# Optimization experiments

Hardware: AMD Instinct MI355X
Metric: run time of the kernel (lower is better)

The kernel has to match this reference:

```python
import jax, jax.numpy as jnp
import numpy as np

B_, N_, DIM, MDIM, H, HID = 8, 1024, 256, 128, 8, 1024
HD = DIM // H      # 32
MHD = MDIM // H    # 16
EPS = 1e-5


def _bn(x, g, b):
    # x: [B, C, L]; BatchNorm1d with batch statistics (training-mode fwd), biased var
    m = x.mean(axis=(0, 2), keepdims=True)
    v = x.var(axis=(0, 2), keepdims=True)
    return (x - m) / jnp.sqrt(v + EPS) * g[None, :, None] + b[None, :, None]


def setup_inputs() -> dict:
    key = jax.random.key(0)
    ks = jax.random.split(key, 12)
    p = lambda k, s: 0.02 * jax.random.normal(k, s, dtype=jnp.float32)
    z = lambda n: jnp.zeros((n,), jnp.float32)
    return {
        "x": jax.random.normal(ks[0], (B_, DIM, N_), dtype=jnp.float32),
        "cor": jax.random.uniform(ks[1], (B_, N_, 3), dtype=jnp.float32),
        "q_w": p(ks[2], (DIM, DIM)),            # qkv_bias=False
        "kv_w": p(ks[3], (2 * DIM, DIM)),
        "cor_w": p(ks[4], (MDIM, 3)),
        "proj_w": p(ks[5], (DIM, DIM)), "proj_b": z(DIM),
        "mproj_w": p(ks[6], (MDIM, MDIM)), "mproj_b": z(MDIM),
        "g1": jnp.ones((DIM,), jnp.float32), "b1": z(DIM),
        "g2": jnp.ones((DIM,), jnp.float32), "b2": z(DIM),
        "fc1_w": p(ks[7], (HID, DIM)), "fc1_b": z(HID),
        "dw_w": 1.0 + p(ks[8], (HID,)), "dw_b": z(HID),  # Conv1d k=1 groups=C -> per-channel affine
        "prelu_a": jnp.array(0.25, jnp.float32),
        "fc2_w": p(ks[9], (DIM, HID)), "fc2_b": z(DIM),
        "N": N_,
        "B": B_,
    }


def reference(x, cor, q_w, kv_w, cor_w, proj_w, proj_b, mproj_w, mproj_b,
              g1, b1, g2, b2, fc1_w, fc1_b, dw_w, dw_b, prelu_a,
              fc2_w, fc2_b, N, B):
    nwB = x.shape[0]
    scale = float(HD) ** -0.5
    # norm1 + to tokens [B, N, C]
    xn = _bn(x, g1, b1).transpose(0, 2, 1)
    # swap batch halves (frame reversal)
    xr = jnp.concatenate([xn[nwB // 2:], xn[:nwB // 2]], axis=0)
    # attention projections
    q = (xn @ q_w.T).reshape(nwB, N_, H, HD).transpose(0, 2, 1, 3)       # [B,H,N,hd]
    kv = (xr @ kv_w.T).reshape(nwB, N_, 2, H, HD).transpose(2, 0, 3, 1, 4)
    k, v = kv[0], kv[1]
    ce = cor @ cor_w.T                                                    # [B,N,M]
    ceh = ce.reshape(nwB, N_, H, MHD).transpose(0, 2, 1, 3)               # [B,H,N,mhd]
    attn = jax.nn.softmax(jnp.einsum('bhnd,bhmd->bhnm', q, k) * scale, axis=-1)
    # attention matrix reused for value and motion paths
    xa = (attn @ v).transpose(0, 2, 1, 3).reshape(nwB, N_, DIM) @ proj_w.T + proj_b
    cr = (attn @ ceh).transpose(0, 2, 1, 3).reshape(nwB, N_, MDIM)
    motion = (cr - ce) @ mproj_w.T + mproj_b
    # residual + norm2 + DWConv-MLP
    xn2 = xn + xa                                                         # [B,N,C]
    xb = _bn(xn2.transpose(0, 2, 1), g2, b2).transpose(0, 2, 1)           # [B,N,C]
    h = xb @ fc1_w.T + fc1_b
    h = h * dw_w + dw_b                                                   # depthwise 1x1 conv
    h = jnp.where(h >= 0, h, prelu_a * h)                                 # PReLU
    out = h @ fc2_w.T + fc2_b
    x_out = x + out.transpose(0, 2, 1)                                    # [B,C,N]
    return (x_out, motion)
```

## Files before the change

### kernel.cpp

```cpp
#include <hip/hip_runtime.h>
#include <hip/hip_bf16.h>
#include <math.h>

#define C_DIM 256
#define N_PTS 1024
#define H_N 8
#define MDIM_N 128
#define HID_N 1024
#define EPSV 1e-5f
#define R_TOT 8192
#define CN 262144

typedef __bf16 bf16x8 __attribute__((ext_vector_type(8)));
typedef __bf16 bf16x4 __attribute__((ext_vector_type(4)));
typedef float f32x4 __attribute__((ext_vector_type(4)));

#define QSCALE 0.25503482f

__device__ inline unsigned short bfu(float f) {
  union { __bf16 h; unsigned short u; } c;
  c.h = (__bf16)f;
  return c.u;
}

__global__ __launch_bounds__(256)
void wcvt_k(const float* __restrict__ s0, const float* __restrict__ s1,
            const float* __restrict__ s2, const float* __restrict__ s3,
            const float* __restrict__ s4, const float* __restrict__ s5,
            __bf16* d0, __bf16* d1, __bf16* d2, __bf16* d3, __bf16* d4,
            __bf16* d5) {
  int i = blockIdx.x * 256 + threadIdx.x;
  const float* s; __bf16* d; int off;
  if      (i <  16384) { s = s0; d = d0; off = 0; }
  else if (i <  49152) { s = s1; d = d1; off = 16384; }
  else if (i <  65536) { s = s2; d = d2; off = 49152; }
  else if (i <  69632) { s = s3; d = d3; off = 65536; }
  else if (i < 135168) { s = s4; d = d4; off = 69632; }
  else                 { s = s5; d = d5; off = 135168; }
  int j = i - off;
  float4 v = ((const float4*)s)[j];
  ushort4 u;
  u.x = bfu(v.x); u.y = bfu(v.y); u.z = bfu(v.z); u.w = bfu(v.w);
  ((ushort4*)d)[j] = u;
}

__global__ __launch_bounds__(256)
void bn1_stats_k(const float* __restrict__ x, const float* __restrict__ g,
                 const float* __restrict__ bb, float* __restrict__ st) {
  int c = blockIdx.x;
  int t = threadIdx.x;
  float s = 0.f, q = 0.f;
  for (int i = 0; i < 32; ++i) {
    int idx = t + i * 256;
    int b = idx >> 10, n = idx & 1023;
    float v = x[(size_t)b * CN + (size_t)c * N_PTS + n];
    s += v; q += v * v;
  }
  __shared__ float ss[256], sq[256];
  ss[t] = s; sq[t] = q;
  __syncthreads();
  for (int off = 128; off > 0; off >>= 1) {
    if (t < off) { ss[t] += ss[t + off]; sq[t] += sq[t + off]; }
    __syncthreads();
  }
  if (t == 0) {
    float mean = ss[0] * (1.f / 8192.f);
    float var  = sq[0] * (1.f / 8192.f) - mean * mean;
    float sc   = g[c] * rsqrtf(var + EPSV);
    st[c]          = sc;
    st[C_DIM + c]  = bb[c] - mean * sc;
  }
}

__global__ __launch_bounds__(256)
void norm1_t_k(const float* __restrict__ x, const float* __restrict__ st,
               float* __restrict__ xn, __bf16* __restrict__ xnb) {
  __shared__ float tile[32][33];
  int c0 = blockIdx.x * 32, n0 = blockIdx.y * 32, b = blockIdx.z;
  int tx = threadIdx.x, ty = threadIdx.y;
#pragma unroll
  for (int k = 0; k < 4; ++k) {
    int ci = ty + k * 8;
    int c = c0 + ci;
    float v = x[(size_t)b * CN + (size_t)c * N_PTS + n0 + tx];
    tile[ci][tx] = v * st[c] + st[C_DIM + c];
  }
  __syncthreads();
#pragma unroll
  for (int k = 0; k < 4; ++k) {
    int ni = ty + k * 8;
    size_t o = ((size_t)(b * N_PTS + n0 + ni)) * C_DIM + c0 + tx;
    float v = tile[tx][ni];
    xn[o] = v;
    xnb[o] = (__bf16)v;
  }
}

__global__ __launch_bounds__(256)
void cet_k(const float* __restrict__ cor, const float* __restrict__ cw,
           __bf16* __restrict__ vt) {
  __shared__ float cs[768];
  int bh = blockIdx.x; int b = bh >> 3, h = bh & 7;
  int n0 = blockIdx.y * 256;
  int t = threadIdx.x;
  for (int i = t; i < 768; i += 256)
    cs[i] = cor[(size_t)(b * N_PTS + n0) * 3 + i];
  __syncthreads();
  int md = t >> 4, ns = (t & 15) * 16;
  float w0 = cw[(h * 16 + md) * 3 + 0];
  float w1 = cw[(h * 16 + md) * 3 + 1];
  float w2 = cw[(h * 16 + md) * 3 + 2];
  __bf16* dst = &vt[((size_t)bh * 48 + 32 + md) * 1024 + n0 + ns];
#pragma unroll
  for (int g2 = 0; g2 < 4; ++g2) {
    ushort4 u;
    float v0 = cs[(ns + g2 * 4 + 0) * 3] * w0 + cs[(ns + g2 * 4 + 0) * 3 + 1] * w1 + cs[(ns + g2 * 4 + 0) * 3 + 2] * w2;
    float v1 = cs[(ns + g2 * 4 + 1) * 3] * w0 + cs[(ns + g2 * 4 + 1) * 3 + 1] * w1 + cs[(ns + g2 * 4 + 1) * 3 + 2] * w2;
    float v2 = cs[(ns + g2 * 4 + 2) * 3] * w0 + cs[(ns + g2 * 4 + 2) * 3 + 1] * w1 + cs[(ns + g2 * 4 + 2) * 3 + 2] * w2;
    float v3 = cs[(ns + g2 * 4 + 3) * 3] * w0 + cs[(ns + g2 * 4 + 3) * 3 + 1] * w1 + cs[(ns + g2 * 4 + 3) * 3 + 2] * w2;
    u.x = bfu(v0); u.y = bfu(v1); u.z = bfu(v2); u.w = bfu(v3);
    *(ushort4*)&dst[g2 * 4] = u;
  }
}

__global__ __launch_bounds__(512)
void attn_k(const __bf16* __restrict__ qb, const __bf16* __restrict__ kb,
            const __bf16* __restrict__ vt, const float* __restrict__ cor,
            const float* __restrict__ cw, __bf16* __restrict__ av,
            __bf16* __restrict__ dmc) {
  __shared__ __bf16 KsV[2][64][40];
  __shared__ __bf16 VtV[2][48][72];
  __shared__ __bf16 Pbuf[8][16][72];

  int bh = blockIdx.x; int b = bh >> 3, h = bh & 7;
  int t = threadIdx.x;
  int w = t >> 6, lane = t & 63;
  int l15 = lane & 15, g = lane >> 4;

  int nloc0 = blockIdx.y * 128 + w * 16;
  bf16x8 aq =
      *(const bf16x8*)&qb[((size_t)bh * N_PTS + nloc0 + l15) * 32 + g * 8];

  const __bf16* ksrc = kb + (size_t)bh * N_PTS * 32;
  const __bf16* vsrc = vt + (size_t)bh * 48 * N_PTS;
  int u = t - 256;
  int vdv = u >> 3, vkg = u & 7;

  float mrun = -1e30f, lrun = 0.f;
  f32x4 acco[3];
#pragma unroll
  for (int mt = 0; mt < 3; ++mt) acco[mt] = (f32x4){0.f, 0.f, 0.f, 0.f};

  if (t < 256) {
    *(uint4*)&KsV[0][t >> 2][(t & 3) * 8] = *(const uint4*)&ksrc[t * 8];
  } else {
    *(uint4*)&VtV[0][vdv][vkg * 8] =
        *(const uint4*)&vsrc[(size_t)vdv * N_PTS + vkg * 8];
    if (u < 128)
      *(uint4*)&VtV[0][32 + vdv][vkg * 8] =
          *(const uint4*)&vsrc[(size_t)(32 + vdv) * N_PTS + vkg * 8];
  }
  __syncthreads();

  for (int kt = 0; kt < 16; ++kt) {
    int cur = kt & 1, nxt = cur ^ 1;
    uint4 kreg, vreg0, vreg1;
    if (kt < 15) {
      int key1 = (kt + 1) * 64;
      if (t < 256) {
        kreg = *(const uint4*)&ksrc[key1 * 32 + t * 8];
      } else {
        vreg0 = *(const uint4*)&vsrc[(size_t)vdv * N_PTS + key1 + vkg * 8];
        if (u < 128)
          vreg1 =
              *(const uint4*)&vsrc[(size_t)(32 + vdv) * N_PTS + key1 + vkg * 8];
      }
    }

    f32x4 sq[4];
    __builtin_amdgcn_s_setprio(1);
#pragma unroll
    for (int nt = 0; nt < 4; ++nt) {
      bf16x8 kf = *(const bf16x8*)&KsV[cur][nt * 16 + l15][g * 8];
      f32x4 z = (f32x4){0.f, 0.f, 0.f, 0.f};
      sq[nt] = __builtin_amdgcn_mfma_f32_16x16x32_bf16(kf, aq, z, 0, 0, 0);
    }
    __builtin_amdgcn_s_setprio(0);

    float tm = fmaxf(fmaxf(fmaxf(sq[0][0], sq[0][1]), fmaxf(sq[0][2], sq[0][3])),
                     fmaxf(fmaxf(sq[1][0], sq[1][1]), fmaxf(sq[1][2], sq[1][3])));
    tm = fmaxf(tm,
               fmaxf(fmaxf(fmaxf(sq[2][0], sq[2][1]), fmaxf(sq[2][2], sq[2][3])),
                     fmaxf(fmaxf(sq[3][0], sq[3][1]), fmaxf(sq[3][2], sq[3][3]))));
    tm = fmaxf(tm, __shfl_xor(tm, 16));
    tm = fmaxf(tm, __shfl_xor(tm, 32));
    float nm = fmaxf(mrun, tm);
    float corr = exp2f(mrun - nm);
    mrun = nm;
    float rs = 0.f;
#pragma unroll
    for (int nt = 0; nt < 4; ++nt)
#pragma unroll
      for (int r = 0; r < 4; ++r) {
        float p = exp2f(sq[nt][r] - nm);
        sq[nt][r] = p;
        rs += p;
      }
    rs += __shfl_xor(rs, 16);
    rs += __shfl_xor(rs, 32);
    lrun = lrun * corr + rs;
#pragma unroll
    for (int mt = 0; mt < 3; ++mt)
#pragma unroll
      for (int r = 0; r < 4; ++r) acco[mt][r] *= corr;

#pragma unroll
    for (int nt = 0; nt < 4; ++nt) {
      bf16x4 pk;
      pk[0] = (__bf16)sq[nt][0]; pk[1] = (__bf16)sq[nt][1];
      pk[2] = (__bf16)sq[nt][2]; pk[3] = (__bf16)sq[nt][3];
      *(bf16x4*)&Pbuf[w][l15][nt * 16 + g * 4] = pk;
    }
    bf16x8 ap[2];
#pragma unroll
    for (int kc = 0; kc < 2; ++kc)
      ap[kc] = *(const bf16x8*)&Pbuf[w][l15][kc * 32 + g * 8];

    __builtin_amdgcn_s_setprio(1);
#pragma unroll
    for (int mt = 0; mt < 3; ++mt)
#pragma unroll
      for (int kc = 0; kc < 2; ++kc) {
        bf16x8 vf = *(const bf16x8*)&VtV[cur][mt * 16 + l15][kc * 32 + g * 8];
        acco[mt] = __builtin_amdgcn_mfma_f32_16x16x32_bf16(vf, ap[kc],
                                                           acco[mt], 0, 0, 0);
      }
    __builtin_amdgcn_s_setprio(0);

    if (kt < 15) {
      if (t < 256) {
        *(uint4*)&KsV[nxt][t >> 2][(t & 3) * 8] = kreg;
      } else {
        *(uint4*)&VtV[nxt][vdv][vkg * 8] = vreg0;
        if (u < 128) *(uint4*)&VtV[nxt][32 + vdv][vkg * 8] = vreg1;
      }
      __syncthreads();
    }
  }

  float inv = 1.f / lrun;
  int row = b * N_PTS + nloc0 + l15;
#pragma unroll
  for (int mt = 0; mt < 2; ++mt) {
    ushort4 o;
    o.x = bfu(acco[mt][0] * inv); o.y = bfu(acco[mt][1] * inv);
    o.z = bfu(acco[mt][2] * inv); o.w = bfu(acco[mt][3] * inv);
    *(ushort4*)&av[(size_t)row * C_DIM + h * 32 + mt * 16 + g * 4] = o;
  }
  {
    const float* cp = &cor[(size_t)row * 3];
    float c0 = cp[0], c1 = cp[1], c2 = cp[2];
    ushort4 o;
#pragma unroll
    for (int r = 0; r < 4; ++r) {
      int md = h * 16 + g * 4 + r;
      float ce = c0 * cw[md * 3] + c1 * cw[md * 3 + 1] + c2 * cw[md * 3 + 2];
      float v = acco[2][r] * inv - ce;
      ((unsigned short*)&o)[r] = bfu(v);
    }
    *(ushort4*)&dmc[(size_t)row * MDIM_N + h * 16 + g * 4] = o;
  }
}

template <int MODE, int BNt>
__global__ __launch_bounds__(256)
void mgemm_k(const __bf16* __restrict__ A, const __bf16* __restrict__ W,
             const float* __restrict__ bias, void* __restrict__ outp,
             const float* __restrict__ e0, const float* __restrict__ e2,
             const float* __restrict__ e3, const float* __restrict__ pre,
             __bf16* __restrict__ kbp, __bf16* __restrict__ vtp,
             float* __restrict__ raw2, int K, int M) {
  constexpr int WN = BNt / 2;
  constexpr int NR = WN / 16;
  __shared__ __bf16 Al[128 * 64];
  __shared__ __bf16 Bl[BNt * 64];
  int t = threadIdx.x;
  int w = t >> 6, lane = t & 63;
  int l15 = lane & 15, g = lane >> 4;
  int wr = w >> 1, wn = w & 1;
  int r0 = blockIdx.y * 128;
  int m0 = blockIdx.x * BNt;
  bool swapA = (MODE == 1) && (m0 >= 256);

  f32x4 acc[4][NR];
#pragma unroll
  for (int i = 0; i < 4; ++i)
#pragma unroll
    for (int j = 0; j < NR; ++j) acc[i][j] = (f32x4){0.f, 0.f, 0.f, 0.f};

  for (int kt = 0; kt < K; kt += 64) {
    __syncthreads();
#pragma unroll
    for (int p = 0; p < 4; ++p) {
      int flat = p * 256 + t;
      int row = flat >> 3, c16 = flat & 7;
      int gr = r0 + row;
      if (swapA) gr = ((((gr >> 10) + 4) & 7) << 10) | (gr & 1023);
      *(uint4*)&Al[row * 64 + (c16 ^ (row & 7)) * 8] =
          *(const uint4*)&A[(size_t)gr * K + kt + c16 * 8];
    }
#pragma unroll
    for (int p = 0; p < BNt / 32; ++p) {
      int flat = p * 256 + t;
      int row = flat >> 3, c16 = flat & 7;
      *(uint4*)&Bl[row * 64 + (c16 ^ (row & 7)) * 8] =
          *(const uint4*)&W[(size_t)(m0 + row) * K + kt + c16 * 8];
    }
    __syncthreads();
#pragma unroll
    for (int ks = 0; ks < 2; ++ks) {
      bf16x8 af[4], bf_[NR];
#pragma unroll
      for (int mf = 0; mf < 4; ++mf) {
        int row = wr * 64 + mf * 16 + l15;
        af[mf] = *(const bf16x8*)&Al[row * 64 + ((ks * 4 + g) ^ (l15 & 7)) * 8];
      }
#pragma unroll
      for (int nf = 0; nf < NR; ++nf) {
        int row = wn * WN + nf * 16 + l15;
        bf_[nf] = *(const bf16x8*)&Bl[row * 64 + ((ks * 4 + g) ^ (l15 & 7)) * 8];
      }
#pragma unroll
      for (int mf = 0; mf < 4; ++mf)
#pragma unroll
        for (int nf = 0; nf < NR; ++nf)
          acc[mf][nf] = __builtin_amdgcn_mfma_f32_16x16x32_bf16(
              af[mf], bf_[nf], acc[mf][nf], 0, 0, 0);
    }
  }

  float a_pre = (MODE == 4) ? pre[0] : 0.f;
  float sS[NR], sQ[NR];
#pragma unroll
  for (int j = 0; j < NR; ++j) { sS[j] = 0.f; sQ[j] = 0.f; }

#pragma unroll
  for (int mf = 0; mf < 4; ++mf) {
#pragma unroll
    for (int nf = 0; nf < NR; ++nf) {
      int m = m0 + wn * WN + nf * 16 + l15;
      int rbase = r0 + wr * 64 + mf * 16 + g * 4;
      if (MODE == 5) {
        int b = rbase >> 10, n = rbase & 1023;
        size_t oi = (size_t)b * CN + (size_t)m * N_PTS + n;
        float4 xv = *(const float4*)&e0[oi];
        float bs = bias[m];
        float4 ov;
        ov.x = xv.x + acc[mf][nf][0] + bs;
        ov.y = xv.y + acc[mf][nf][1] + bs;
        ov.z = xv.z + acc[mf][nf][2] + bs;
        ov.w = xv.w + acc[mf][nf][3] + bs;
        *(float4*)&((float*)outp)[oi] = ov;
      } else if (MODE == 1 && m0 >= 512) {
        int d = m - 512, hh = d >> 5, dd = d & 31;
        int b = rbase >> 10, n0v = rbase & 1023;
        ushort4 uu;
        uu.x = bfu(acc[mf][nf][0]); uu.y = bfu(acc[mf][nf][1]);
        uu.z = bfu(acc[mf][nf][2]); uu.w = bfu(acc[mf][nf][3]);
        *(ushort4*)&vtp[(((size_t)b * 8 + hh) * 48 + dd) * 1024 + n0v] = uu;
      } else {
#pragma unroll
        for (int r = 0; r < 4; ++r) {
          float v = acc[mf][nf][r];
          if (MODE == 1) {
            int b = rbase >> 10, n = (rbase & 1023) + r;
            if (m0 < 256) {
              int hh = m >> 5, dd = m & 31;
              ((__bf16*)outp)[(((size_t)b * 8 + hh) * 1024 + n) * 32 + dd] =
                  (__bf16)(v * QSCALE);
            } else {
              int d = m - 256, hh = d >> 5, dd = d & 31;
              kbp[(((size_t)b * 8 + hh) * 1024 + n) * 32 + dd] = (__bf16)v;
            }
          } else if (MODE == 2) {
            size_t oi = (size_t)(rbase + r) * M + m;
            float vv = e0[oi] + v + bias[m];
            ((float*)outp)[oi] = vv;
            sS[nf] += vv;
            sQ[nf] += vv * vv;
          } else if (MODE == 3) {
            ((float*)outp)[(size_t)(rbase + r) * M + m] = v + bias[m];
          } else if (MODE == 4) {
            v += bias[m];
            v = v * e2[m] + e3[m];
            ((__bf16*)outp)[(size_t)(rbase + r) * M + m] =
                (__bf16)(v >= 0.f ? v : a_pre * v);
          }
        }
      }
    }
  }

  if (MODE == 2) {
    __syncthreads();
    float* colS = (float*)&Al[0];
    float* colQ = colS + BNt;
    if (t < 2 * BNt) colS[t] = 0.f;
    __syncthreads();
#pragma unroll
    for (int nf = 0; nf < NR; ++nf) {
      int mc = wn * WN + nf * 16 + l15;
      atomicAdd(&colS[mc], sS[nf]);
      atomicAdd(&colQ[mc], sQ[nf]);
    }
    __syncthreads();
    if (t < BNt) {
      atomicAdd(&raw2[m0 + t], colS[t]);
      atomicAdd(&raw2[256 + m0 + t], colQ[t]);
    }
  }
}

__global__ __launch_bounds__(256)
void bn2af_k(const float* __restrict__ xn2, const float* __restrict__ raw,
             const float* __restrict__ g, const float* __restrict__ bb,
             __bf16* __restrict__ xb) {
  __shared__ float sts[256], sth[256];
  int t = threadIdx.x;
  {
    float mean = raw[t] * (1.f / 8192.f);
    float var  = raw[256 + t] * (1.f / 8192.f) - mean * mean;
    float sc   = g[t] * rsqrtf(var + EPSV);
    sts[t] = sc;
    sth[t] = bb[t] - mean * sc;
  }
  __syncthreads();
  int i = blockIdx.x * 256 + t;
  float4 v = ((const float4*)xn2)[i];
  int c = (i * 4) & 255;
  ushort4 u;
  u.x = bfu(v.x * sts[c]     + sth[c]);
  u.y = bfu(v.y * sts[c + 1] + sth[c + 1]);
  u.z = bfu(v.z * sts[c + 2] + sth[c + 2]);
  u.w = bfu(v.w * sts[c + 3] + sth[c + 3]);
  ((ushort4*)xb)[i] = u;
}

extern "C" void kernel_launch(void* const* d_in, const int* in_sizes, int n_in,
                              void* d_out, int out_size, void* d_ws,
                              size_t ws_size, hipStream_t stream) {
  const float* x       = (const float*)d_in[0];
  const float* cor     = (const float*)d_in[1];
  const float* q_w     = (const float*)d_in[2];
  const float* kv_w    = (const float*)d_in[3];
  const float* cor_w   = (const float*)d_in[4];
  const float* proj_w  = (const float*)d_in[5];
  const float* proj_b  = (const float*)d_in[6];
  const float* mproj_w = (const float*)d_in[7];
  const float* mproj_b = (const float*)d_in[8];
  const float* g1      = (const float*)d_in[9];
  const float* b1      = (const float*)d_in[10];
  const float* g2      = (const float*)d_in[11];
  const float* b2      = (const float*)d_in[12];
  const float* fc1_w   = (const float*)d_in[13];
  const float* fc1_b   = (const float*)d_in[14];
  const float* dw_w    = (const float*)d_in[15];
  const float* dw_b    = (const float*)d_in[16];
  const float* prelu   = (const float*)d_in[17];
  const float* fc2_w   = (const float*)d_in[18];
  const float* fc2_b   = (const float*)d_in[19];

  char* base = (char*)d_ws;
  const size_t MB = 1u << 20;
  float*  xn32 = (float*)(base + 0);
  __bf16* xnb  = (__bf16*)(base + 8 * MB);
  __bf16* qb   = (__bf16*)(base + 12 * MB);
  __bf16* kb   = (__bf16*)(base + 16 * MB);
  __bf16* vt   = (__bf16*)(base + 20 * MB);
  __bf16* av   = (__bf16*)(base + 30 * MB);
  __bf16* dmc  = (__bf16*)(base + 34 * MB);
  float*  xn2  = (float*)(base + 36 * MB);
  __bf16* xb   = (__bf16*)(base + 8 * MB);
  __bf16* hb   = (__bf16*)(base + 12 * MB);
  __bf16* qwb  = (__bf16*)(base + 44 * MB);
  __bf16* kvwb = (__bf16*)(base + 44 * MB + 131072);
  __bf16* pwb  = (__bf16*)(base + 44 * MB + 393216);
  __bf16* mwb  = (__bf16*)(base + 44 * MB + 524288);
  __bf16* f1wb = (__bf16*)(base + 44 * MB + 557056);
  __bf16* f2wb = (__bf16*)(base + 44 * MB + 1081344);
  float*  raw2 = (float*)(base + 45 * MB + 655360);
  float*  st1  = raw2 + 1024;
  float* out0 = (float*)d_out;
  float* out1 = out0 + 2097152;

  (void)hipMemsetAsync(raw2, 0, 512 * sizeof(float), stream);

  wcvt_k<<<784, 256, 0, stream>>>(q_w, kv_w, proj_w, mproj_w, fc1_w, fc2_w,
                                  qwb, kvwb, pwb, mwb, f1wb, f2wb);
  bn1_stats_k<<<256, 256, 0, stream>>>(x, g1, b1, st1);
  norm1_t_k<<<dim3(8, 32, 8), dim3(32, 8), 0, stream>>>(x, st1, xn32, xnb);

  mgemm_k<1, 128><<<dim3(6, 64), 256, 0, stream>>>(
      xnb, qwb, nullptr, qb, nullptr, nullptr, nullptr, nullptr, kb, vt,
      nullptr, 256, 768);
  cet_k<<<dim3(64, 4), 256, 0, stream>>>(cor, cor_w, vt);

  attn_k<<<dim3(64, 8), 512, 0, stream>>>(qb, kb, vt, cor, cor_w, av, dmc);

  mgemm_k<2, 64><<<dim3(4, 64), 256, 0, stream>>>(
      av, pwb, proj_b, xn2, xn32, nullptr, nullptr, nullptr, nullptr, nullptr,
      raw2, 256, 256);
  mgemm_k<3, 64><<<dim3(2, 64), 256, 0, stream>>>(
      dmc, mwb, mproj_b, out1, nullptr, nullptr, nullptr, nullptr, nullptr,
      nullptr, nullptr, 128, 128);

  bn2af_k<<<2048, 256, 0, stream>>>(xn2, raw2, g2, b2, xb);

  mgemm_k<4, 128><<<dim3(8, 64), 256, 0, stream>>>(
      xb, f1wb, fc1_b, hb, nullptr, dw_w, dw_b, prelu, nullptr, nullptr,
      nullptr, 256, HID_N);
  mgemm_k<5, 64><<<dim3(4, 64), 256, 0, stream>>>(
      hb, f2wb, fc2_b, out0, x, nullptr, nullptr, nullptr, nullptr, nullptr,
      nullptr, HID_N, 256);
}
```

Before: 119.3 us.

## Fuse prep kernels, merge proj/motion GEMMs, fold BN2 into fc1 loader

```diff
diff --git a/kernel.cpp b/kernel.cpp
--- a/kernel.cpp
+++ b/kernel.cpp
@@ -24,57 +24,82 @@
 }
 
 __global__ __launch_bounds__(256)
-void wcvt_k(const float* __restrict__ s0, const float* __restrict__ s1,
+void prep_k(const float* __restrict__ s0, const float* __restrict__ s1,
             const float* __restrict__ s2, const float* __restrict__ s3,
             const float* __restrict__ s4, const float* __restrict__ s5,
             __bf16* d0, __bf16* d1, __bf16* d2, __bf16* d3, __bf16* d4,
-            __bf16* d5) {
-  int i = blockIdx.x * 256 + threadIdx.x;
-  const float* s; __bf16* d; int off;
-  if      (i <  16384) { s = s0; d = d0; off = 0; }
-  else if (i <  49152) { s = s1; d = d1; off = 16384; }
-  else if (i <  65536) { s = s2; d = d2; off = 49152; }
-  else if (i <  69632) { s = s3; d = d3; off = 65536; }
-  else if (i < 135168) { s = s4; d = d4; off = 69632; }
-  else                 { s = s5; d = d5; off = 135168; }
-  int j = i - off;
-  float4 v = ((const float4*)s)[j];
-  ushort4 u;
-  u.x = bfu(v.x); u.y = bfu(v.y); u.z = bfu(v.z); u.w = bfu(v.w);
-  ((ushort4*)d)[j] = u;
-}
-
-__global__ __launch_bounds__(256)
-void bn1_stats_k(const float* __restrict__ x, const float* __restrict__ g,
-                 const float* __restrict__ bb, float* __restrict__ st) {
-  int c = blockIdx.x;
+            __bf16* d5, const float* __restrict__ cor,
+            const float* __restrict__ cw, __bf16* __restrict__ vt,
+            const float* __restrict__ x, const float* __restrict__ g1,
+            const float* __restrict__ b1, float* __restrict__ st) {
+  int blk = blockIdx.x;
   int t = threadIdx.x;
-  float s = 0.f, q = 0.f;
-  for (int i = 0; i < 32; ++i) {
-    int idx = t + i * 256;
-    int b = idx >> 10, n = idx & 1023;
-    float v = x[(size_t)b * CN + (size_t)c * N_PTS + n];
-    s += v; q += v * v;
-  }
-  __shared__ float ss[256], sq[256];
-  ss[t] = s; sq[t] = q;
-  __syncthreads();
-  for (int off = 128; off > 0; off >>= 1) {
-    if (t < off) { ss[t] += ss[t + off]; sq[t] += sq[t + off]; }
-    __syncthreads();
-  }
-  if (t == 0) {
-    float mean = ss[0] * (1.f / 8192.f);
-    float var  = sq[0] * (1.f / 8192.f) - mean * mean;
-    float sc   = g[c] * rsqrtf(var + EPSV);
-    st[c]          = sc;
-    st[C_DIM + c]  = bb[c] - mean * sc;
+  if (blk < 784) {
+    int i = blk * 256 + t;
+    const float* s; __bf16* d; int off;
+    if      (i <  16384) { s = s0; d = d0; off = 0; }
+    else if (i <  49152) { s = s1; d = d1; off = 16384; }
+    else if (i <  65536) { s = s2; d = d2; off = 49152; }
+    else if (i <  69632) { s = s3; d = d3; off = 65536; }
+    else if (i < 135168) { s = s4; d = d4; off = 69632; }
+    else                 { s = s5; d = d5; off = 135168; }
+    int j = i - off;
+    float4 v = ((const float4*)s)[j];
+    ushort4 u;
+    u.x = bfu(v.x); u.y = bfu(v.y); u.z = bfu(v.z); u.w = bfu(v.w);
+    ((ushort4*)d)[j] = u;
+  } else if (blk < 1040) {
+    __shared__ float cs[768];
+    int j = blk - 784;
+    int bh = j & 63, b = bh >> 3, h = bh & 7;
+    int n0 = (j >> 6) * 256;
+    for (int i = t; i < 768; i += 256)
+      cs[i] = cor[(size_t)(b * N_PTS + n0) * 3 + i];
+    __syncthreads();
+    int md = t >> 4, ns = (t & 15) * 16;
+    float w0 = cw[(h * 16 + md) * 3 + 0];
+    float w1 = cw[(h * 16 + md) * 3 + 1];
+    float w2 = cw[(h * 16 + md) * 3 + 2];
+    __bf16* dst = &vt[((size_t)bh * 48 + 32 + md) * 1024 + n0 + ns];
+#pragma unroll
+    for (int g2 = 0; g2 < 4; ++g2) {
+      ushort4 u;
+      float v0 = cs[(ns + g2 * 4 + 0) * 3] * w0 + cs[(ns + g2 * 4 + 0) * 3 + 1] * w1 + cs[(ns + g2 * 4 + 0) * 3 + 2] * w2;
+      float v1 = cs[(ns + g2 * 4 + 1) * 3] * w0 + cs[(ns + g2 * 4 + 1) * 3 + 1] * w1 + cs[(ns + g2 * 4 + 1) * 3 + 2] * w2;
+      float v2 = cs[(ns + g2 * 4 + 2) * 3] * w0 + cs[(ns + g2 * 4 + 2) * 3 + 1] * w1 + cs[(ns + g2 * 4 + 2) * 3 + 2] * w2;
+      float v3 = cs[(ns + g2 * 4 + 3) * 3] * w0 + cs[(ns + g2 * 4 + 3) * 3 + 1] * w1 + cs[(ns + g2 * 4 + 3) * 3 + 2] * w2;
+      u.x = bfu(v0); u.y = bfu(v1); u.z = bfu(v2); u.w = bfu(v3);
+      *(ushort4*)&dst[g2 * 4] = u;
+    }
+  } else {
+    __shared__ float ss[256], sq[256];
+    int c = blk - 1040;
+    float s = 0.f, q = 0.f;
+    for (int i = 0; i < 32; ++i) {
+      int idx = t + i * 256;
+      int b = idx >> 10, n = idx & 1023;
+      float v = x[(size_t)b * CN + (size_t)c * N_PTS + n];
+      s += v; q += v * v;
+    }
+    ss[t] = s; sq[t] = q;
+    __syncthreads();
+    for (int off = 128; off > 0; off >>= 1) {
+      if (t < off) { ss[t] += ss[t + off]; sq[t] += sq[t + off]; }
+      __syncthreads();
+    }
+    if (t == 0) {
+      float mean = ss[0] * (1.f / 8192.f);
+      float var  = sq[0] * (1.f / 8192.f) - mean * mean;
+      float sc   = g1[c] * rsqrtf(var + EPSV);
+      st[c]          = sc;
+      st[C_DIM + c]  = b1[c] - mean * sc;
+    }
   }
 }
 
 __global__ __launch_bounds__(256)
 void norm1_t_k(const float* __restrict__ x, const float* __restrict__ st,
-               float* __restrict__ xn, __bf16* __restrict__ xnb) {
+               __bf16* __restrict__ xnb) {
   __shared__ float tile[32][33];
   int c0 = blockIdx.x * 32, n0 = blockIdx.y * 32, b = blockIdx.z;
   int tx = threadIdx.x, ty = threadIdx.y;
@@ -89,37 +114,8 @@
 #pragma unroll
   for (int k = 0; k < 4; ++k) {
     int ni = ty + k * 8;
-    size_t o = ((size_t)(b * N_PTS + n0 + ni)) * C_DIM + c0 + tx;
-    float v = tile[tx][ni];
-    xn[o] = v;
-    xnb[o] = (__bf16)v;
-  }
-}
-
-__global__ __launch_bounds__(256)
-void cet_k(const float* __restrict__ cor, const float* __restrict__ cw,
-           __bf16* __restrict__ vt) {
-  __shared__ float cs[768];
-  int bh = blockIdx.x; int b = bh >> 3, h = bh & 7;
-  int n0 = blockIdx.y * 256;
-  int t = threadIdx.x;
-  for (int i = t; i < 768; i += 256)
-    cs[i] = cor[(size_t)(b * N_PTS + n0) * 3 + i];
-  __syncthreads();
-  int md = t >> 4, ns = (t & 15) * 16;
-  float w0 = cw[(h * 16 + md) * 3 + 0];
-  float w1 = cw[(h * 16 + md) * 3 + 1];
-  float w2 = cw[(h * 16 + md) * 3 + 2];
-  __bf16* dst = &vt[((size_t)bh * 48 + 32 + md) * 1024 + n0 + ns];
-#pragma unroll
-  for (int g2 = 0; g2 < 4; ++g2) {
-    ushort4 u;
-    float v0 = cs[(ns + g2 * 4 + 0) * 3] * w0 + cs[(ns + g2 * 4 + 0) * 3 + 1] * w1 + cs[(ns + g2 * 4 + 0) * 3 + 2] * w2;
-    float v1 = cs[(ns + g2 * 4 + 1) * 3] * w0 + cs[(ns + g2 * 4 + 1) * 3 + 1] * w1 + cs[(ns + g2 * 4 + 1) * 3 + 2] * w2;
-    float v2 = cs[(ns + g2 * 4 + 2) * 3] * w0 + cs[(ns + g2 * 4 + 2) * 3 + 1] * w1 + cs[(ns + g2 * 4 + 2) * 3 + 2] * w2;
-    float v3 = cs[(ns + g2 * 4 + 3) * 3] * w0 + cs[(ns + g2 * 4 + 3) * 3 + 1] * w1 + cs[(ns + g2 * 4 + 3) * 3 + 2] * w2;
-    u.x = bfu(v0); u.y = bfu(v1); u.z = bfu(v2); u.w = bfu(v3);
-    *(ushort4*)&dst[g2 * 4] = u;
+    xnb[((size_t)(b * N_PTS + n0 + ni)) * C_DIM + c0 + tx] =
+        (__bf16)tile[tx][ni];
   }
 }
 
@@ -276,10 +272,8 @@
 __global__ __launch_bounds__(256)
 void mgemm_k(const __bf16* __restrict__ A, const __bf16* __restrict__ W,
              const float* __restrict__ bias, void* __restrict__ outp,
-             const float* __restrict__ e0, const float* __restrict__ e2,
-             const float* __restrict__ e3, const float* __restrict__ pre,
-             __bf16* __restrict__ kbp, __bf16* __restrict__ vtp,
-             float* __restrict__ raw2, int K, int M) {
+             const float* __restrict__ e0, __bf16* __restrict__ kbp,
+             __bf16* __restrict__ vtp, int K, int M) {
   constexpr int WN = BNt / 2;
   constexpr int NR = WN / 16;
   __shared__ __bf16 Al[128 * 64];
@@ -338,11 +332,6 @@
               af[mf], bf_[nf], acc[mf][nf], 0, 0, 0);
     }
   }
-
-  float a_pre = (MODE == 4) ? pre[0] : 0.f;
-  float sS[NR], sQ[NR];
-#pragma unroll
-  for (int j = 0; j < NR; ++j) { sS[j] = 0.f; sQ[j] = 0.f; }
 
 #pragma unroll
   for (int mf = 0; mf < 4; ++mf) {
@@ -372,49 +361,123 @@
 #pragma unroll
         for (int r = 0; r < 4; ++r) {
           float v = acc[mf][nf][r];
-          if (MODE == 1) {
-            int b = rbase >> 10, n = (rbase & 1023) + r;
-            if (m0 < 256) {
-              int hh = m >> 5, dd = m & 31;
-              ((__bf16*)outp)[(((size_t)b * 8 + hh) * 1024 + n) * 32 + dd] =
-                  (__bf16)(v * QSCALE);
-            } else {
-              int d = m - 256, hh = d >> 5, dd = d & 31;
-              kbp[(((size_t)b * 8 + hh) * 1024 + n) * 32 + dd] = (__bf16)v;
-            }
-          } else if (MODE == 2) {
-            size_t oi = (size_t)(rbase + r) * M + m;
-            float vv = e0[oi] + v + bias[m];
-            ((float*)outp)[oi] = vv;
-            sS[nf] += vv;
-            sQ[nf] += vv * vv;
-          } else if (MODE == 3) {
-            ((float*)outp)[(size_t)(rbase + r) * M + m] = v + bias[m];
-          } else if (MODE == 4) {
-            v += bias[m];
-            v = v * e2[m] + e3[m];
-            ((__bf16*)outp)[(size_t)(rbase + r) * M + m] =
-                (__bf16)(v >= 0.f ? v : a_pre * v);
+          int b = rbase >> 10, n = (rbase & 1023) + r;
+          if (m0 < 256) {
+            int hh = m >> 5, dd = m & 31;
+            ((__bf16*)outp)[(((size_t)b * 8 + hh) * 1024 + n) * 32 + dd] =
+                (__bf16)(v * QSCALE);
+          } else {
+            int d = m - 256, hh = d >> 5, dd = d & 31;
+            kbp[(((size_t)b * 8 + hh) * 1024 + n) * 32 + dd] = (__bf16)v;
           }
         }
       }
     }
   }
-
-  if (MODE == 2) {
+}
+
+__global__ __launch_bounds__(256)
+void projmot_k(const __bf16* __restrict__ av, const __bf16* __restrict__ pw,
+               const float* __restrict__ pb, float* __restrict__ xn2,
+               const __bf16* __restrict__ xnb, const __bf16* __restrict__ dmc,
+               const __bf16* __restrict__ mw, const float* __restrict__ mb,
+               float* __restrict__ mot, float* __restrict__ raw2) {
+  __shared__ __bf16 Al[128 * 64];
+  __shared__ __bf16 Bl[64 * 64];
+  bool isProj = blockIdx.x < 4;
+  const __bf16* A = isProj ? av : dmc;
+  const __bf16* W = isProj ? pw : mw;
+  const float* bias = isProj ? pb : mb;
+  int K = isProj ? 256 : 128;
+  int m0 = (isProj ? blockIdx.x : (blockIdx.x - 4)) * 64;
+  int t = threadIdx.x;
+  int w = t >> 6, lane = t & 63;
+  int l15 = lane & 15, g = lane >> 4;
+  int wr = w >> 1, wn = w & 1;
+  int r0 = blockIdx.y * 128;
+
+  f32x4 acc[4][2];
+#pragma unroll
+  for (int i = 0; i < 4; ++i)
+#pragma unroll
+    for (int j = 0; j < 2; ++j) acc[i][j] = (f32x4){0.f, 0.f, 0.f, 0.f};
+
+  for (int kt = 0; kt < K; kt += 64) {
+    __syncthreads();
+#pragma unroll
+    for (int p = 0; p < 4; ++p) {
+      int flat = p * 256 + t;
+      int row = flat >> 3, c16 = flat & 7;
+      *(uint4*)&Al[row * 64 + (c16 ^ (row & 7)) * 8] =
+          *(const uint4*)&A[(size_t)(r0 + row) * K + kt + c16 * 8];
+    }
+#pragma unroll
+    for (int p = 0; p < 2; ++p) {
+      int flat = p * 256 + t;
+      int row = flat >> 3, c16 = flat & 7;
+      *(uint4*)&Bl[row * 64 + (c16 ^ (row & 7)) * 8] =
+          *(const uint4*)&W[(size_t)(m0 + row) * K + kt + c16 * 8];
+    }
+    __syncthreads();
+#pragma unroll
+    for (int ks = 0; ks < 2; ++ks) {
+      bf16x8 af[4], bf_[2];
+#pragma unroll
+      for (int mf = 0; mf < 4; ++mf) {
+        int row = wr * 64 + mf * 16 + l15;
+        af[mf] = *(const bf16x8*)&Al[row * 64 + ((ks * 4 + g) ^ (l15 & 7)) * 8];
+      }
+#pragma unroll
+      for (int nf = 0; nf < 2; ++nf) {
+        int row = wn * 32 + nf * 16 + l15;
+        bf_[nf] = *(const bf16x8*)&Bl[row * 64 + ((ks * 4 + g) ^ (l15 & 7)) * 8];
+      }
+#pragma unroll
+      for (int mf = 0; mf < 4; ++mf)
+#pragma unroll
+        for (int nf = 0; nf < 2; ++nf)
+          acc[mf][nf] = __builtin_amdgcn_mfma_f32_16x16x32_bf16(
+              af[mf], bf_[nf], acc[mf][nf], 0, 0, 0);
+    }
+  }
+
+  float sS[2] = {0.f, 0.f}, sQ[2] = {0.f, 0.f};
+#pragma unroll
+  for (int mf = 0; mf < 4; ++mf) {
+#pragma unroll
+    for (int nf = 0; nf < 2; ++nf) {
+      int m = m0 + wn * 32 + nf * 16 + l15;
+      int rbase = r0 + wr * 64 + mf * 16 + g * 4;
+#pragma unroll
+      for (int r = 0; r < 4; ++r) {
+        float v = acc[mf][nf][r];
+        if (isProj) {
+          size_t oi = (size_t)(rbase + r) * C_DIM + m;
+          float vv = (float)xnb[oi] + v + bias[m];
+          xn2[oi] = vv;
+          sS[nf] += vv;
+          sQ[nf] += vv * vv;
+        } else {
+          mot[(size_t)(rbase + r) * MDIM_N + m] = v + bias[m];
+        }
+      }
+    }
+  }
+
+  if (isProj) {
     __syncthreads();
     float* colS = (float*)&Al[0];
-    float* colQ = colS + BNt;
-    if (t < 2 * BNt) colS[t] = 0.f;
-    __syncthreads();
-#pragma unroll
-    for (int nf = 0; nf < NR; ++nf) {
-      int mc = wn * WN + nf * 16 + l15;
+    float* colQ = colS + 64;
+    if (t < 128) colS[t] = 0.f;
+    __syncthreads();
+#pragma unroll
+    for (int nf = 0; nf < 2; ++nf) {
+      int mc = wn * 32 + nf * 16 + l15;
       atomicAdd(&colS[mc], sS[nf]);
       atomicAdd(&colQ[mc], sQ[nf]);
     }
     __syncthreads();
-    if (t < BNt) {
+    if (t < 64) {
       atomicAdd(&raw2[m0 + t], colS[t]);
       atomicAdd(&raw2[256 + m0 + t], colQ[t]);
     }
@@ -422,28 +485,108 @@
 }
 
 __global__ __launch_bounds__(256)
-void bn2af_k(const float* __restrict__ xn2, const float* __restrict__ raw,
-             const float* __restrict__ g, const float* __restrict__ bb,
-             __bf16* __restrict__ xb) {
-  __shared__ float sts[256], sth[256];
+void fc1_k(const float* __restrict__ xn2, const float* __restrict__ raw2,
+           const float* __restrict__ g2, const float* __restrict__ b2,
+           const __bf16* __restrict__ W, const float* __restrict__ bias,
+           const float* __restrict__ dw_w, const float* __restrict__ dw_b,
+           const float* __restrict__ pre, __bf16* __restrict__ hb) {
+  __shared__ __bf16 Al[128 * 64];
+  __shared__ __bf16 Bl[128 * 64];
+  __shared__ float scs[256], shs[256];
   int t = threadIdx.x;
+  int w = t >> 6, lane = t & 63;
+  int l15 = lane & 15, g = lane >> 4;
+  int wr = w >> 1, wn = w & 1;
+  int r0 = blockIdx.y * 128;
+  int m0 = blockIdx.x * 128;
+
   {
-    float mean = raw[t] * (1.f / 8192.f);
-    float var  = raw[256 + t] * (1.f / 8192.f) - mean * mean;
-    float sc   = g[t] * rsqrtf(var + EPSV);
-    sts[t] = sc;
-    sth[t] = bb[t] - mean * sc;
+    float mean = raw2[t] * (1.f / 8192.f);
+    float var  = raw2[256 + t] * (1.f / 8192.f) - mean * mean;
+    float sc   = g2[t] * rsqrtf(var + EPSV);
+    scs[t] = sc;
+    shs[t] = b2[t] - mean * sc;
   }
   __syncthreads();
-  int i = blockIdx.x * 256 + t;
-  float4 v = ((const float4*)xn2)[i];
-  int c = (i * 4) & 255;
-  ushort4 u;
-  u.x = bfu(v.x * sts[c]     + sth[c]);
-  u.y = bfu(v.y * sts[c + 1] + sth[c + 1]);
-  u.z = bfu(v.z * sts[c + 2] + sth[c + 2]);
-  u.w = bfu(v.w * sts[c + 3] + sth[c + 3]);
-  ((ushort4*)xb)[i] = u;
+
+  f32x4 acc[4][4];
+#pragma unroll
+  for (int i = 0; i < 4; ++i)
+#pragma unroll
+    for (int j = 0; j < 4; ++j) acc[i][j] = (f32x4){0.f, 0.f, 0.f, 0.f};
+
+  for (int kt = 0; kt < 256; kt += 64) {
+    __syncthreads();
+#pragma unroll
+    for (int p = 0; p < 4; ++p) {
+      int flat = p * 256 + t;
+      int row = flat >> 3, c16 = flat & 7;
+      int k = kt + c16 * 8;
+      const float* src = &xn2[(size_t)(r0 + row) * C_DIM + k];
+      float4 v0 = *(const float4*)src;
+      float4 v1 = *(const float4*)(src + 4);
+      float4 s0 = *(const float4*)&scs[k];
+      float4 s1 = *(const float4*)&scs[k + 4];
+      float4 h0 = *(const float4*)&shs[k];
+      float4 h1 = *(const float4*)&shs[k + 4];
+      bf16x8 a;
+      a[0] = (__bf16)(v0.x * s0.x + h0.x);
+      a[1] = (__bf16)(v0.y * s0.y + h0.y);
+      a[2] = (__bf16)(v0.z * s0.z + h0.z);
+      a[3] = (__bf16)(v0.w * s0.w + h0.w);
+      a[4] = (__bf16)(v1.x * s1.x + h1.x);
+      a[5] = (__bf16)(v1.y * s1.y + h1.y);
+      a[6] = (__bf16)(v1.z * s1.z + h1.z);
+      a[7] = (__bf16)(v1.w * s1.w + h1.w);
+      *(bf16x8*)&Al[row * 64 + (c16 ^ (row & 7)) * 8] = a;
+    }
+#pragma unroll
+    for (int p = 0; p < 4; ++p) {
+      int flat = p * 256 + t;
+      int row = flat >> 3, c16 = flat & 7;
+      *(uint4*)&Bl[row * 64 + (c16 ^ (row & 7)) * 8] =
+          *(const uint4*)&W[(size_t)(m0 + row) * 256 + kt + c16 * 8];
+    }
+    __syncthreads();
+#pragma unroll
+    for (int ks = 0; ks < 2; ++ks) {
+      bf16x8 af[4], bf_[4];
+#pragma unroll
+      for (int mf = 0; mf < 4; ++mf) {
+        int row = wr * 64 + mf * 16 + l15;
+        af[mf] = *(const bf16x8*)&Al[row * 64 + ((ks * 4 + g) ^ (l15 & 7)) * 8];
+      }
+#pragma unroll
+      for (int nf = 0; nf < 4; ++nf) {
+        int row = wn * 64 + nf * 16 + l15;
+        bf_[nf] = *(const bf16x8*)&Bl[row * 64 + ((ks * 4 + g) ^ (l15 & 7)) * 8];
+      }
+#pragma unroll
+      for (int mf = 0; mf < 4; ++mf)
+#pragma unroll
+        for (int nf = 0; nf < 4; ++nf)
+          acc[mf][nf] = __builtin_amdgcn_mfma_f32_16x16x32_bf16(
+              af[mf], bf_[nf], acc[mf][nf], 0, 0, 0);
+    }
+  }
+
+  float a_pre = pre[0];
+#pragma unroll
+  for (int mf = 0; mf < 4; ++mf) {
+#pragma unroll
+    for (int nf = 0; nf < 4; ++nf) {
+      int m = m0 + wn * 64 + nf * 16 + l15;
+      int rbase = r0 + wr * 64 + mf * 16 + g * 4;
+      float bs = bias[m], dwm = dw_w[m], dbm = dw_b[m];
+#pragma unroll
+      for (int r = 0; r < 4; ++r) {
+        float v = acc[mf][nf][r] + bs;
+        v = v * dwm + dbm;
+        hb[(size_t)(rbase + r) * HID_N + m] =
+            (__bf16)(v >= 0.f ? v : a_pre * v);
+      }
+    }
+  }
 }
 
 extern "C" void kernel_launch(void* const* d_in, const int* in_sizes, int n_in,
@@ -472,7 +615,6 @@
 
   char* base = (char*)d_ws;
   const size_t MB = 1u << 20;
-  float*  xn32 = (float*)(base + 0);
   __bf16* xnb  = (__bf16*)(base + 8 * MB);
   __bf16* qb   = (__bf16*)(base + 12 * MB);
   __bf16* kb   = (__bf16*)(base + 16 * MB);
@@ -480,7 +622,6 @@
   __bf16* av   = (__bf16*)(base + 30 * MB);
   __bf16* dmc  = (__bf16*)(base + 34 * MB);
   float*  xn2  = (float*)(base + 36 * MB);
-  __bf16* xb   = (__bf16*)(base + 8 * MB);
   __bf16* hb   = (__bf16*)(base + 12 * MB);
   __bf16* qwb  = (__bf16*)(base + 44 * MB);
   __bf16* kvwb = (__bf16*)(base + 44 * MB + 131072);
@@ -495,31 +636,22 @@
 
   (void)hipMemsetAsync(raw2, 0, 512 * sizeof(float), stream);
 
-  wcvt_k<<<784, 256, 0, stream>>>(q_w, kv_w, proj_w, mproj_w, fc1_w, fc2_w,
-                                  qwb, kvwb, pwb, mwb, f1wb, f2wb);
-  bn1_stats_k<<<256, 256, 0, stream>>>(x, g1, b1, st1);
-  norm1_t_k<<<dim3(8, 32, 8), dim3(32, 8), 0, stream>>>(x, st1, xn32, xnb);
+  prep_k<<<1296, 256, 0, stream>>>(q_w, kv_w, proj_w, mproj_w, fc1_w, fc2_w,
+                                   qwb, kvwb, pwb, mwb, f1wb, f2wb,
+                                   cor, cor_w, vt, x, g1, b1, st1);
+  norm1_t_k<<<dim3(8, 32, 8), dim3(32, 8), 0, stream>>>(x, st1, xnb);
 
   mgemm_k<1, 128><<<dim3(6, 64), 256, 0, stream>>>(
-      xnb, qwb, nullptr, qb, nullptr, nullptr, nullptr, nullptr, kb, vt,
-      nullptr, 256, 768);
-  cet_k<<<dim3(64, 4), 256, 0, stream>>>(cor, cor_w, vt);
+      xnb, qwb, nullptr, qb, nullptr, kb, vt, 256, 768);
 
   attn_k<<<dim3(64, 8), 512, 0, stream>>>(qb, kb, vt, cor, cor_w, av, dmc);
 
-  mgemm_k<2, 64><<<dim3(4, 64), 256, 0, stream>>>(
-      av, pwb, proj_b, xn2, xn32, nullptr, nullptr, nullptr, nullptr, nullptr,
-      raw2, 256, 256);
-  mgemm_k<3, 64><<<dim3(2, 64), 256, 0, stream>>>(
-      dmc, mwb, mproj_b, out1, nullptr, nullptr, nullptr, nullptr, nullptr,
-      nullptr, nullptr, 128, 128);
-
-  bn2af_k<<<2048, 256, 0, stream>>>(xn2, raw2, g2, b2, xb);
-
-  mgemm_k<4, 128><<<dim3(8, 64), 256, 0, stream>>>(
-      xb, f1wb, fc1_b, hb, nullptr, dw_w, dw_b, prelu, nullptr, nullptr,
-      nullptr, 256, HID_N);
+  projmot_k<<<dim3(6, 64), 256, 0, stream>>>(av, pwb, proj_b, xn2, xnb,
+                                             dmc, mwb, mproj_b, out1, raw2);
+
+  fc1_k<<<dim3(8, 64), 256, 0, stream>>>(xn2, raw2, g2, b2, f1wb, fc1_b,
+                                         dw_w, dw_b, prelu, hb);
+
   mgemm_k<5, 64><<<dim3(4, 64), 256, 0, stream>>>(
-      hb, f2wb, fc2_b, out0, x, nullptr, nullptr, nullptr, nullptr, nullptr,
-      nullptr, HID_N, 256);
-}
+      hb, f2wb, fc2_b, out0, x, nullptr, nullptr, HID_N, 256);
+}
```

After: 123.5 us. 3.5% more time.
